# Performance work log

Hardware: AMD Instinct MI355X
Metric: run time of the kernel (lower is better)

The kernel has to match this reference:

```python
import jax, jax.numpy as jnp
import numpy as np

D_MODEL = 1024
NUM_HEADS = 16
D_K = D_MODEL // NUM_HEADS
B, S = 2, 2048


def setup_inputs() -> dict:
    key = jax.random.key(0)
    ks = jax.random.split(key, 11)
    lim = 1.0 / np.sqrt(D_MODEL)  # torch Linear default init range
    def lin(kw, kb):
        W = jax.random.uniform(kw, (D_MODEL, D_MODEL), jnp.float32, -lim, lim)
        b = jax.random.uniform(kb, (D_MODEL,), jnp.float32, -lim, lim)
        return W, b
    Wq, bq = lin(ks[0], ks[1])
    Wk, bk = lin(ks[2], ks[3])
    Wv, bv = lin(ks[4], ks[5])
    Wo, bo = lin(ks[6], ks[7])
    return {
        "Q": jax.random.normal(ks[8], (B, S, D_MODEL), jnp.float32),
        "K": jax.random.normal(ks[9], (B, S, D_MODEL), jnp.float32),
        "V": jax.random.normal(ks[10], (B, S, D_MODEL), jnp.float32),
        "Wq": Wq, "bq": bq, "Wk": Wk, "bk": bk,
        "Wv": Wv, "bv": bv, "Wo": Wo, "bo": bo,
        "validate": False,
    }


def _split_heads(x):
    b, s, _ = x.shape
    return x.reshape(b, s, NUM_HEADS, D_K).transpose(0, 2, 1, 3)  # [B,H,S,Dk]


def reference(Q, K, V, Wq, bq, Wk, bk, Wv, bv, Wo, bo, validate):
    # Linear projections (torch Linear: x @ W.T + b)
    q = _split_heads(Q @ Wq.T + bq)
    k = _split_heads(K @ Wk.T + bk)
    v = _split_heads(V @ Wv.T + bv)
    scale = 1.0 / jnp.sqrt(jnp.asarray(D_K, q.dtype))
    scores = jnp.einsum("bhqd,bhkd->bhqk", q, k) * scale  # [B,H,S,S]
    attn = jax.nn.softmax(scores, axis=-1)
    out = jnp.einsum("bhqk,bhkd->bhqd", attn, v)  # [B,H,S,Dk]
    out = out.transpose(0, 2, 1, 3).reshape(Q.shape[0], Q.shape[1], D_MODEL)
    return out @ Wo.T + bo
```

## Files before the change

### kernel.cpp

```cpp
#include <hip/hip_runtime.h>


typedef short bf16x8 __attribute__((ext_vector_type(8)));
typedef float f32x4 __attribute__((ext_vector_type(4)));

#define D_MODEL 1024
#define NHEAD 16
#define DK 64
#define BB 2
#define SS 2048
#define MROWS (BB * SS)
#define C1 0.18033688011112042f

__device__ __forceinline__ unsigned short f2bf(float f) {
  unsigned u = __builtin_bit_cast(unsigned, f);
  u += 0x7fffu + ((u >> 16) & 1u);
  return (unsigned short)(u >> 16);
}
__device__ __forceinline__ unsigned pack2(float a, float b) {
  return (unsigned)f2bf(a) | ((unsigned)f2bf(b) << 16);
}
__device__ __forceinline__ unsigned cvtpk(float lo, float hi) {
  unsigned r;
  asm("v_cvt_pk_bf16_f32 %0, %1, %2" : "=v"(r) : "v"(lo), "v"(hi));
  return r;
}
__device__ __forceinline__ float max3f(float a, float b, float c) {
  float d;
  asm("v_max3_f32 %0, %1, %2, %3" : "=v"(d) : "v"(a), "v"(b), "v"(c));
  return d;
}

typedef __attribute__((address_space(3))) unsigned int as3u;
typedef const __attribute__((address_space(1))) unsigned int as1u;
__device__ __forceinline__ void gload16(void* lds, const void* g) {
  __builtin_amdgcn_global_load_lds((as1u*)g, (as3u*)lds, 16, 0, 0);
}
__device__ __forceinline__ void waitv16() { asm volatile("s_waitcnt vmcnt(16)" ::: "memory"); }
__device__ __forceinline__ void waitv8()  { asm volatile("s_waitcnt vmcnt(8)"  ::: "memory"); }
__device__ __forceinline__ void waitv4()  { asm volatile("s_waitcnt vmcnt(4)"  ::: "memory"); }
__device__ __forceinline__ void waitv0()  { asm volatile("s_waitcnt vmcnt(0)"  ::: "memory"); }

struct CvtArgs {
  const float* s[7];
  unsigned short* d[7];
  int n8[7];
};

__global__ __launch_bounds__(256) void convert_bf16(CvtArgs a) {
  const int slot = blockIdx.y;
  const float* __restrict__ s = a.s[slot];
  unsigned short* __restrict__ d = a.d[slot];
  const int n8 = a.n8[slot];
  for (int i = blockIdx.x * 256 + threadIdx.x; i < n8; i += gridDim.x * 256) {
    const size_t off = (size_t)i * 8;
    const float4 v0 = *(const float4*)&s[off];
    const float4 v1 = *(const float4*)&s[off + 4];
    uint4 p;
    p.x = pack2(v0.x, v0.y); p.y = pack2(v0.z, v0.w);
    p.z = pack2(v1.x, v1.y); p.w = pack2(v1.z, v1.w);
    *(uint4*)&d[off] = p;
  }
}

template <int MODE>
__device__ __forceinline__ void gemm128(unsigned short* smem,
                                        const unsigned short* __restrict__ A,
                                        const unsigned short* __restrict__ B,
                                        const float* __restrict__ bias,
                                        float scale, int bm, int nb,
                                        float* __restrict__ Cf,
                                        unsigned short* __restrict__ Cb) {
  const int BUF = 2 * 128 * 64;
  const int tid = threadIdx.x;
  const int lane = tid & 63, w = tid >> 6;
  const int wm = w >> 1, wn = w & 1;
  const int l15 = lane & 15, l4 = lane >> 4;

  auto stage = [&](int slot, int k0) {
    unsigned short* As = smem + slot * BUF;
    unsigned short* Bs = As + 128 * 64;
#pragma unroll
    for (int i = 0; i < 4; ++i) {
      const int flat = i * 256 + tid;
      const int row = flat >> 3, g = flat & 7;
      const int gs = (g ^ (row & 7)) << 3;
      gload16(&As[flat * 8], &A[(size_t)(bm * 128 + row) * D_MODEL + k0 + gs]);
    }
#pragma unroll
    for (int i = 0; i < 4; ++i) {
      const int flat = i * 256 + tid;
      const int row = flat >> 3, g = flat & 7;
      const int gs = (g ^ (row & 7)) << 3;
      gload16(&Bs[flat * 8], &B[(size_t)(nb * 128 + row) * D_MODEL + k0 + gs]);
    }
  };

  f32x4 acc[4][4];
#pragma unroll
  for (int m = 0; m < 4; ++m)
#pragma unroll
    for (int n = 0; n < 4; ++n) acc[m][n] = (f32x4){0.f, 0.f, 0.f, 0.f};

  stage(0, 0);
  stage(1, 64);
#pragma unroll
  for (int t = 0; t < 16; ++t) {
    if (t + 2 < 16) stage((t + 2) % 3, (t + 2) * 64);
    if (t < 14) waitv16();
    else if (t == 14) waitv8();
    else waitv0();
    __builtin_amdgcn_s_barrier();
    unsigned short* As = smem + (t % 3) * BUF;
    unsigned short* Bs = As + 128 * 64;
#pragma unroll
    for (int kk = 0; kk < 2; ++kk) {
      bf16x8 af[4], bf[4];
#pragma unroll
      for (int m = 0; m < 4; ++m) {
        const int r = wm * 64 + m * 16 + l15;
        af[m] = *(const bf16x8*)&As[r * 64 + (((kk * 4 + l4) ^ (r & 7)) << 3)];
      }
#pragma unroll
      for (int n = 0; n < 4; ++n) {
        const int r = wn * 64 + n * 16 + l15;
        bf[n] = *(const bf16x8*)&Bs[r * 64 + (((kk * 4 + l4) ^ (r & 7)) << 3)];
      }
#pragma unroll
      for (int m = 0; m < 4; ++m)
#pragma unroll
        for (int n = 0; n < 4; ++n)
          acc[m][n] = __builtin_amdgcn_mfma_f32_16x16x32_bf16(af[m], bf[n], acc[m][n], 0, 0, 0);
    }
    __builtin_amdgcn_s_barrier();
  }

  if (MODE != 2) {
#pragma unroll
    for (int m = 0; m < 4; ++m)
#pragma unroll
      for (int n = 0; n < 4; ++n) {
        const int col = nb * 128 + wn * 64 + n * 16 + l15;
        const float bv = bias[col];
#pragma unroll
        for (int r = 0; r < 4; ++r) {
          const int row = bm * 128 + wm * 64 + m * 16 + l4 * 4 + r;
          const float v = (acc[m][n][r] + bv) * scale;
          if (MODE == 0) Cb[(size_t)row * D_MODEL + col] = f2bf(v);
          else           Cf[(size_t)row * D_MODEL + col] = v;
        }
      }
  } else {
    unsigned short* T = smem;
#pragma unroll
    for (int m = 0; m < 4; ++m)
#pragma unroll
      for (int n = 0; n < 4; ++n) {
        const int cl = wn * 64 + n * 16 + l15;
        const float bv = bias[nb * 128 + cl];
#pragma unroll
        for (int r = 0; r < 4; ++r) {
          const int rl = wm * 64 + m * 16 + l4 * 4 + r;
          const int byte = cl * 256 + ((((rl >> 3) ^ (cl & 7))) << 4) + ((rl & 7) << 1);
          *(unsigned short*)((char*)T + byte) = f2bf(acc[m][n][r] + bv);
        }
      }
    __syncthreads();
#pragma unroll
    for (int c = 0; c < 8; ++c) {
      const int chunk = c * 256 + tid;
      const int cl = chunk >> 4, rl0 = (chunk & 15) * 8;
      const int byte = cl * 256 + (((rl0 >> 3) ^ (cl & 7)) << 4);
      const uint4 val = *(const uint4*)((const char*)T + byte);
      const int gcol = nb * 128 + cl;
      const int bb = (bm * 128) >> 11;
      const int s = ((bm * 128) & 2047) + rl0;
      *(uint4*)&Cb[(size_t)(bb * 1024 + gcol) * SS + s] = val;
    }
  }
}

__global__ __launch_bounds__(256, 1) void gemm_qkv(
    const unsigned short* __restrict__ Xq, const unsigned short* __restrict__ Xk,
    const unsigned short* __restrict__ Xv,
    const unsigned short* __restrict__ Wq, const float* __restrict__ bq,
    const unsigned short* __restrict__ Wk, const float* __restrict__ bk,
    const unsigned short* __restrict__ Wv, const float* __restrict__ bv,
    unsigned short* __restrict__ q, unsigned short* __restrict__ k,
    unsigned short* __restrict__ vT) {
  __shared__ __align__(16) unsigned short smem[3 * 2 * 128 * 64];
  const int lin = blockIdx.x + 24 * blockIdx.y;
  const int swz = (lin % 8) * 96 + lin / 8;
  const int bn = swz % 24, bm = swz / 24;
  const int z = bn >> 3, nb = bn & 7;
  if (z < 2) {
    const unsigned short* X = z ? Xk : Xq;
    const unsigned short* W = z ? Wk : Wq;
    const float* bi = z ? bk : bq;
    unsigned short* O = z ? k : q;
    gemm128<0>(smem, X, W, bi, z ? 1.0f : C1, bm, nb, nullptr, O);
  } else {
    gemm128<2>(smem, Xv, Wv, bv, 1.0f, bm, nb, nullptr, vT);
  }
}

__global__ __launch_bounds__(256, 1) void gemm_o(const unsigned short* __restrict__ A,
                                                 const unsigned short* __restrict__ W,
                                                 const float* __restrict__ bi,
                                                 float* __restrict__ out) {
  __shared__ __align__(16) unsigned short smem[3 * 2 * 128 * 64];
  const int lin = blockIdx.x + 8 * blockIdx.y;
  const int swz = (lin % 8) * 32 + lin / 8;
  const int bn = swz % 8, bm = swz / 8;
  gemm128<1>(smem, A, W, bi, 1.0f, bm, bn, out, nullptr);
}

__global__ __launch_bounds__(256, 2) void attn_kernel(
    const unsigned short* __restrict__ Qp, const unsigned short* __restrict__ Kp,
    const unsigned short* __restrict__ vTp, unsigned short* __restrict__ Op) {
  __shared__ __align__(16) unsigned short Kt[3][64 * 64];
  __shared__ __align__(16) unsigned short Vt[3][64 * 64];
  __shared__ __align__(16) unsigned short Pt[4][32 * 64];
  const int tid = threadIdx.x;
  const int lane = tid & 63, w = tid >> 6;
  const int l15 = lane & 15, l4 = lane >> 4;
  const int bh = blockIdx.x;
  const int b = bh >> 4, h = bh & 15;
  const int qb = blockIdx.y;
  const size_t baseQ = (size_t)b * SS * D_MODEL + (size_t)h * DK;
  const size_t baseV = (size_t)(b * 1024 + h * 64) * SS;

  bf16x8 aq[2][2];
#pragma unroll
  for (int m = 0; m < 2; ++m) {
    const int qrow = qb * 128 + w * 32 + m * 16 + l15;
#pragma unroll
    for (int kk = 0; kk < 2; ++kk)
      aq[m][kk] = *(const bf16x8*)&Qp[baseQ + (size_t)qrow * D_MODEL + kk * 32 + l4 * 8];
  }

  const bf16x8 vone = {0x3F80, 0x3F80, 0x3F80, 0x3F80, 0x3F80, 0x3F80, 0x3F80, 0x3F80};

  float rm[2] = {-1e30f, -1e30f};
  f32x4 acc[2][5];
#pragma unroll
  for (int m = 0; m < 2; ++m)
#pragma unroll
    for (int d = 0; d < 5; ++d) acc[m][d] = (f32x4){0.f, 0.f, 0.f, 0.f};

  auto stage = [&](int buf, int kt) {
#pragma unroll
    for (int i = 0; i < 2; ++i) {
      const int flat = (w * 2 + i) * 64 + lane;
      const int row = flat >> 3, g = flat & 7;
      gload16(&Kt[buf][flat * 8],
              &Kp[baseQ + (size_t)(kt * 64 + row) * D_MODEL + ((g ^ (row & 7)) << 3)]);
    }
#pragma unroll
    for (int i = 0; i < 2; ++i) {
      const int flat = (w * 2 + i) * 64 + lane;
      const int row = flat >> 3, g = flat & 7;
      gload16(&Vt[buf][flat * 8],
              &vTp[baseV + (size_t)row * SS + kt * 64 + ((g ^ (row & 7)) << 3)]);
    }
  };

  stage(0, 0);
  stage(1, 1);
#pragma unroll 1
  for (int kt = 0; kt < SS / 64; ++kt) {
    const int bs = kt % 3;
    if (kt < SS / 64 - 2) {
      int bst = bs + 2; if (bst >= 3) bst -= 3;
      stage(bst, kt + 2);
    }
    if (kt < SS / 64 - 2) waitv8();
    else if (kt == SS / 64 - 2) waitv4();
    else waitv0();
    __builtin_amdgcn_s_barrier();

    f32x4 st[2][4];
#pragma unroll
    for (int m = 0; m < 2; ++m)
#pragma unroll
      for (int n = 0; n < 4; ++n) st[m][n] = (f32x4){0.f, 0.f, 0.f, 0.f};
#pragma unroll
    for (int kk = 0; kk < 2; ++kk) {
      bf16x8 kf[4];
#pragma unroll
      for (int n = 0; n < 4; ++n) {
        const int r = n * 16 + l15;
        kf[n] = *(const bf16x8*)&Kt[bs][r * 64 + (((kk * 4 + l4) ^ (r & 7)) << 3)];
      }
#pragma unroll
      for (int m = 0; m < 2; ++m)
#pragma unroll
        for (int n = 0; n < 4; ++n)
          st[m][n] = __builtin_amdgcn_mfma_f32_16x16x32_bf16(kf[n], aq[m][kk], st[m][n], 0, 0, 0);
    }

    float mx[2];
#pragma unroll
    for (int m = 0; m < 2; ++m) {
      const float a0 = max3f(st[m][0][0], st[m][0][1], st[m][0][2]);
      const float a1 = max3f(st[m][0][3], st[m][1][0], st[m][1][1]);
      const float a2 = max3f(st[m][1][2], st[m][1][3], st[m][2][0]);
      const float a3 = max3f(st[m][2][1], st[m][2][2], st[m][2][3]);
      const float a4 = max3f(st[m][3][0], st[m][3][1], st[m][3][2]);
      float v = fmaxf(max3f(a0, a1, a2), max3f(a3, a4, st[m][3][3]));
      v = fmaxf(v, __shfl_xor(v, 16));
      v = fmaxf(v, __shfl_xor(v, 32));
      mx[m] = v;
    }
    if (__any((mx[0] > rm[0] + 8.f) | (mx[1] > rm[1] + 8.f))) {
#pragma unroll
      for (int m = 0; m < 2; ++m) {
        const float nm = fmaxf(rm[m], mx[m]);
        const float alpha = exp2f(rm[m] - nm);
        rm[m] = nm;
#pragma unroll
        for (int r = 0; r < 4; ++r) {
          const float ar = __shfl(alpha, l4 * 4 + r);
#pragma unroll
          for (int d = 0; d < 5; ++d) acc[m][d][r] *= ar;
        }
      }
    }
#pragma unroll
    for (int m = 0; m < 2; ++m)
#pragma unroll
      for (int n = 0; n < 4; ++n)
#pragma unroll
        for (int r = 0; r < 4; ++r) st[m][n][r] = exp2f(st[m][n][r] - rm[m]);

#pragma unroll
    for (int m = 0; m < 2; ++m)
#pragma unroll
      for (int n = 0; n < 4; ++n)
#pragma unroll
        for (int c = 0; c < 2; ++c) {
          const int col = n * 16 + l4 * 4 + 2 * c;
          const int row = m * 16 + l15;
          const int sw = (((col >> 3) ^ (row & 7)) << 3) + (col & 7);
          *(unsigned*)&Pt[w][row * 64 + sw] = cvtpk(st[m][n][2 * c], st[m][n][2 * c + 1]);
        }

#pragma unroll
    for (int kk = 0; kk < 2; ++kk) {
      bf16x8 ap[2], vf[4];
#pragma unroll
      for (int m = 0; m < 2; ++m) {
        const int r = m * 16 + l15;
        ap[m] = *(const bf16x8*)&Pt[w][r * 64 + (((kk * 4 + l4) ^ (r & 7)) << 3)];
      }
#pragma unroll
      for (int d = 0; d < 4; ++d) {
        const int r = d * 16 + l15;
        vf[d] = *(const bf16x8*)&Vt[bs][r * 64 + (((kk * 4 + l4) ^ (r & 7)) << 3)];
      }
#pragma unroll
      for (int m = 0; m < 2; ++m) {
#pragma unroll
        for (int d = 0; d < 4; ++d)
          acc[m][d] = __builtin_amdgcn_mfma_f32_16x16x32_bf16(ap[m], vf[d], acc[m][d], 0, 0, 0);
        acc[m][4] = __builtin_amdgcn_mfma_f32_16x16x32_bf16(ap[m], vone, acc[m][4], 0, 0, 0);
      }
    }

    __builtin_amdgcn_s_barrier();
  }

#pragma unroll
  for (int m = 0; m < 2; ++m) {
    float inv[4];
#pragma unroll
    for (int r = 0; r < 4; ++r) inv[r] = 1.0f / acc[m][4][r];
#pragma unroll
    for (int d = 0; d < 4; ++d)
#pragma unroll
      for (int r = 0; r < 4; ++r) {
        const int orow = qb * 128 + w * 32 + m * 16 + l4 * 4 + r;
        Op[baseQ + (size_t)orow * D_MODEL + d * 16 + l15] = f2bf(acc[m][d][r] * inv[r]);
      }
  }
}

extern "C" void kernel_launch(void* const* d_in, const int* in_sizes, int n_in,
                              void* d_out, int out_size, void* d_ws, size_t ws_size,
                              hipStream_t stream) {
  const float* Qin = (const float*)d_in[0];
  const float* Kin = (const float*)d_in[1];
  const float* Vin = (const float*)d_in[2];
  const float* Wq = (const float*)d_in[3];
  const float* bq = (const float*)d_in[4];
  const float* Wk = (const float*)d_in[5];
  const float* bk = (const float*)d_in[6];
  const float* Wv = (const float*)d_in[7];
  const float* bv = (const float*)d_in[8];
  const float* Wo = (const float*)d_in[9];
  const float* bo = (const float*)d_in[10];
  float* out = (float*)d_out;

  const size_t NX = (size_t)MROWS * D_MODEL;
  const size_t NW = (size_t)D_MODEL * D_MODEL;
  unsigned short* ws = (unsigned short*)d_ws;
  unsigned short* q  = ws;
  unsigned short* k  = ws + NX;
  unsigned short* vT = ws + 2 * NX;
  unsigned short* Xq = ws + 3 * NX;
  unsigned short* Xk = ws + 4 * NX;
  unsigned short* Xv = ws + 5 * NX;
  unsigned short* wq = ws + 6 * NX;
  unsigned short* wk = wq + NW;
  unsigned short* wv = wk + NW;
  unsigned short* wo = wv + NW;
  unsigned short* ao = Xq;

  CvtArgs ca;
  ca.s[0] = Qin; ca.d[0] = Xq; ca.n8[0] = (int)(NX / 8);
  ca.s[1] = Kin; ca.d[1] = Xk; ca.n8[1] = (int)(NX / 8);
  ca.s[2] = Vin; ca.d[2] = Xv; ca.n8[2] = (int)(NX / 8);
  ca.s[3] = Wq;  ca.d[3] = wq; ca.n8[3] = (int)(NW / 8);
  ca.s[4] = Wk;  ca.d[4] = wk; ca.n8[4] = (int)(NW / 8);
  ca.s[5] = Wv;  ca.d[5] = wv; ca.n8[5] = (int)(NW / 8);
  ca.s[6] = Wo;  ca.d[6] = wo; ca.n8[6] = (int)(NW / 8);
  convert_bf16<<<dim3(1024, 7), 256, 0, stream>>>(ca);

  gemm_qkv<<<dim3(24, 32), 256, 0, stream>>>(
      Xq, Xk, Xv, wq, bq, wk, bk, wv, bv, q, k, vT);
  attn_kernel<<<dim3(BB * NHEAD, SS / 128), 256, 0, stream>>>(q, k, vT, ao);
  gemm_o<<<dim3(8, 32), 256, 0, stream>>>(ao, wo, bo, out);
}
```

Baseline: 237.3 us.

## Fuse fp32-to-bf16 activation conversion into QKV GEMM A-tile loads

```diff
diff --git a/kernel.cpp b/kernel.cpp
--- a/kernel.cpp
+++ b/kernel.cpp
@@ -36,22 +36,20 @@
 __device__ __forceinline__ void gload16(void* lds, const void* g) {
   __builtin_amdgcn_global_load_lds((as1u*)g, (as3u*)lds, 16, 0, 0);
 }
-__device__ __forceinline__ void waitv16() { asm volatile("s_waitcnt vmcnt(16)" ::: "memory"); }
 __device__ __forceinline__ void waitv8()  { asm volatile("s_waitcnt vmcnt(8)"  ::: "memory"); }
 __device__ __forceinline__ void waitv4()  { asm volatile("s_waitcnt vmcnt(4)"  ::: "memory"); }
 __device__ __forceinline__ void waitv0()  { asm volatile("s_waitcnt vmcnt(0)"  ::: "memory"); }
 
 struct CvtArgs {
-  const float* s[7];
-  unsigned short* d[7];
-  int n8[7];
+  const float* s[4];
+  unsigned short* d[4];
 };
 
-__global__ __launch_bounds__(256) void convert_bf16(CvtArgs a) {
+__global__ __launch_bounds__(256) void convert_w(CvtArgs a) {
   const int slot = blockIdx.y;
   const float* __restrict__ s = a.s[slot];
   unsigned short* __restrict__ d = a.d[slot];
-  const int n8 = a.n8[slot];
+  const int n8 = (D_MODEL * D_MODEL) / 8;
   for (int i = blockIdx.x * 256 + threadIdx.x; i < n8; i += gridDim.x * 256) {
     const size_t off = (size_t)i * 8;
     const float4 v0 = *(const float4*)&s[off];
@@ -64,37 +62,47 @@
 }
 
 template <int MODE>
-__device__ __forceinline__ void gemm128(unsigned short* smem,
-                                        const unsigned short* __restrict__ A,
-                                        const unsigned short* __restrict__ B,
-                                        const float* __restrict__ bias,
-                                        float scale, int bm, int nb,
-                                        float* __restrict__ Cf,
-                                        unsigned short* __restrict__ Cb) {
+__device__ __forceinline__ void gemm_qkv_core(unsigned short* smem,
+                                              const float* __restrict__ A,
+                                              const unsigned short* __restrict__ B,
+                                              const float* __restrict__ bias,
+                                              float scale, int bm, int nb,
+                                              unsigned short* __restrict__ Cb) {
   const int BUF = 2 * 128 * 64;
   const int tid = threadIdx.x;
   const int lane = tid & 63, w = tid >> 6;
   const int wm = w >> 1, wn = w & 1;
   const int l15 = lane & 15, l4 = lane >> 4;
 
-  auto stage = [&](int slot, int k0) {
-    unsigned short* As = smem + slot * BUF;
-    unsigned short* Bs = As + 128 * 64;
+  auto stageW = [&](unsigned short* Bs, int k0) {
 #pragma unroll
     for (int i = 0; i < 4; ++i) {
       const int flat = i * 256 + tid;
       const int row = flat >> 3, g = flat & 7;
-      const int gs = (g ^ (row & 7)) << 3;
-      gload16(&As[flat * 8], &A[(size_t)(bm * 128 + row) * D_MODEL + k0 + gs]);
-    }
+      gload16(&Bs[flat * 8], &B[(size_t)(nb * 128 + row) * D_MODEL + k0 + ((g ^ (row & 7)) << 3)]);
+    }
+  };
+  auto loadA = [&](float4 (&ar)[4][2], int k0) {
 #pragma unroll
     for (int i = 0; i < 4; ++i) {
       const int flat = i * 256 + tid;
       const int row = flat >> 3, g = flat & 7;
-      const int gs = (g ^ (row & 7)) << 3;
-      gload16(&Bs[flat * 8], &B[(size_t)(nb * 128 + row) * D_MODEL + k0 + gs]);
+      const float* src = &A[(size_t)(bm * 128 + row) * D_MODEL + k0 + g * 8];
+      ar[i][0] = *(const float4*)src;
+      ar[i][1] = *(const float4*)(src + 4);
     }
   };
+  auto writeA = [&](unsigned short* As, float4 (&ar)[4][2]) {
+#pragma unroll
+    for (int i = 0; i < 4; ++i) {
+      const int flat = i * 256 + tid;
+      const int row = flat >> 3, g = flat & 7;
+      uint4 p;
+      p.x = cvtpk(ar[i][0].x, ar[i][0].y); p.y = cvtpk(ar[i][0].z, ar[i][0].w);
+      p.z = cvtpk(ar[i][1].x, ar[i][1].y); p.w = cvtpk(ar[i][1].z, ar[i][1].w);
+      *(uint4*)&As[row * 64 + ((g ^ (row & 7)) << 3)] = p;
+    }
+  };
 
   f32x4 acc[4][4];
 #pragma unroll
@@ -102,17 +110,24 @@
 #pragma unroll
     for (int n = 0; n < 4; ++n) acc[m][n] = (f32x4){0.f, 0.f, 0.f, 0.f};
 
-  stage(0, 0);
-  stage(1, 64);
-#pragma unroll
+  float4 ar[4][2];
+  stageW(smem + 128 * 64, 0);
+  loadA(ar, 0);
+  waitv0();
+  writeA(smem, ar);
+  __syncthreads();
+
+  int cur = 0;
+#pragma unroll 1
   for (int t = 0; t < 16; ++t) {
-    if (t + 2 < 16) stage((t + 2) % 3, (t + 2) * 64);
-    if (t < 14) waitv16();
-    else if (t == 14) waitv8();
-    else waitv0();
-    __builtin_amdgcn_s_barrier();
-    unsigned short* As = smem + (t % 3) * BUF;
+    unsigned short* As = smem + cur * BUF;
     unsigned short* Bs = As + 128 * 64;
+    unsigned short* Asn = smem + (cur ^ 1) * BUF;
+    const bool more = (t + 1 < 16);
+    if (more) {
+      stageW(Asn + 128 * 64, (t + 1) * 64);
+      loadA(ar, (t + 1) * 64);
+    }
 #pragma unroll
     for (int kk = 0; kk < 2; ++kk) {
       bf16x8 af[4], bf[4];
@@ -132,10 +147,15 @@
         for (int n = 0; n < 4; ++n)
           acc[m][n] = __builtin_amdgcn_mfma_f32_16x16x32_bf16(af[m], bf[n], acc[m][n], 0, 0, 0);
     }
-    __builtin_amdgcn_s_barrier();
-  }
-
-  if (MODE != 2) {
+    if (more) {
+      waitv0();
+      writeA(Asn, ar);
+    }
+    __syncthreads();
+    cur ^= 1;
+  }
+
+  if (MODE == 0) {
 #pragma unroll
     for (int m = 0; m < 4; ++m)
 #pragma unroll
@@ -145,9 +165,7 @@
 #pragma unroll
         for (int r = 0; r < 4; ++r) {
           const int row = bm * 128 + wm * 64 + m * 16 + l4 * 4 + r;
-          const float v = (acc[m][n][r] + bv) * scale;
-          if (MODE == 0) Cb[(size_t)row * D_MODEL + col] = f2bf(v);
-          else           Cf[(size_t)row * D_MODEL + col] = v;
+          Cb[(size_t)row * D_MODEL + col] = f2bf((acc[m][n][r] + bv) * scale);
         }
       }
   } else {
@@ -180,39 +198,112 @@
   }
 }
 
-__global__ __launch_bounds__(256, 1) void gemm_qkv(
-    const unsigned short* __restrict__ Xq, const unsigned short* __restrict__ Xk,
-    const unsigned short* __restrict__ Xv,
+__global__ __launch_bounds__(256, 2) void gemm_qkv(
+    const float* __restrict__ Qin, const float* __restrict__ Kin,
+    const float* __restrict__ Vin,
     const unsigned short* __restrict__ Wq, const float* __restrict__ bq,
     const unsigned short* __restrict__ Wk, const float* __restrict__ bk,
     const unsigned short* __restrict__ Wv, const float* __restrict__ bv,
     unsigned short* __restrict__ q, unsigned short* __restrict__ k,
     unsigned short* __restrict__ vT) {
-  __shared__ __align__(16) unsigned short smem[3 * 2 * 128 * 64];
+  __shared__ __align__(16) unsigned short smem[2 * 2 * 128 * 64];
   const int lin = blockIdx.x + 24 * blockIdx.y;
   const int swz = (lin % 8) * 96 + lin / 8;
   const int bn = swz % 24, bm = swz / 24;
   const int z = bn >> 3, nb = bn & 7;
-  if (z < 2) {
-    const unsigned short* X = z ? Xk : Xq;
-    const unsigned short* W = z ? Wk : Wq;
-    const float* bi = z ? bk : bq;
-    unsigned short* O = z ? k : q;
-    gemm128<0>(smem, X, W, bi, z ? 1.0f : C1, bm, nb, nullptr, O);
+  if (z == 0) {
+    gemm_qkv_core<0>(smem, Qin, Wq, bq, C1, bm, nb, q);
+  } else if (z == 1) {
+    gemm_qkv_core<0>(smem, Kin, Wk, bk, 1.0f, bm, nb, k);
   } else {
-    gemm128<2>(smem, Xv, Wv, bv, 1.0f, bm, nb, nullptr, vT);
-  }
-}
-
-__global__ __launch_bounds__(256, 1) void gemm_o(const unsigned short* __restrict__ A,
+    gemm_qkv_core<2>(smem, Vin, Wv, bv, 1.0f, bm, nb, vT);
+  }
+}
+
+__global__ __launch_bounds__(256, 2) void gemm_o(const unsigned short* __restrict__ A,
                                                  const unsigned short* __restrict__ W,
                                                  const float* __restrict__ bi,
                                                  float* __restrict__ out) {
-  __shared__ __align__(16) unsigned short smem[3 * 2 * 128 * 64];
+  __shared__ __align__(16) unsigned short smem[2 * 2 * 128 * 64];
+  const int BUF = 2 * 128 * 64;
   const int lin = blockIdx.x + 8 * blockIdx.y;
   const int swz = (lin % 8) * 32 + lin / 8;
-  const int bn = swz % 8, bm = swz / 8;
-  gemm128<1>(smem, A, W, bi, 1.0f, bm, bn, out, nullptr);
+  const int nb = swz % 8, bm = swz / 8;
+  const int tid = threadIdx.x;
+  const int lane = tid & 63, w = tid >> 6;
+  const int wm = w >> 1, wn = w & 1;
+  const int l15 = lane & 15, l4 = lane >> 4;
+
+  auto stage = [&](unsigned short* dst, int k0) {
+    unsigned short* As = dst;
+    unsigned short* Bs = dst + 128 * 64;
+#pragma unroll
+    for (int i = 0; i < 4; ++i) {
+      const int flat = i * 256 + tid;
+      const int row = flat >> 3, g = flat & 7;
+      const int gs = (g ^ (row & 7)) << 3;
+      gload16(&As[flat * 8], &A[(size_t)(bm * 128 + row) * D_MODEL + k0 + gs]);
+    }
+#pragma unroll
+    for (int i = 0; i < 4; ++i) {
+      const int flat = i * 256 + tid;
+      const int row = flat >> 3, g = flat & 7;
+      const int gs = (g ^ (row & 7)) << 3;
+      gload16(&Bs[flat * 8], &W[(size_t)(nb * 128 + row) * D_MODEL + k0 + gs]);
+    }
+  };
+
+  f32x4 acc[4][4];
+#pragma unroll
+  for (int m = 0; m < 4; ++m)
+#pragma unroll
+    for (int n = 0; n < 4; ++n) acc[m][n] = (f32x4){0.f, 0.f, 0.f, 0.f};
+
+  stage(smem, 0);
+  int cur = 0;
+#pragma unroll 1
+  for (int t = 0; t < 16; ++t) {
+    if (t + 1 < 16) stage(smem + (cur ^ 1) * BUF, (t + 1) * 64);
+    if (t + 1 < 16) waitv8();
+    else waitv0();
+    __builtin_amdgcn_s_barrier();
+    unsigned short* As = smem + cur * BUF;
+    unsigned short* Bs = As + 128 * 64;
+#pragma unroll
+    for (int kk = 0; kk < 2; ++kk) {
+      bf16x8 af[4], bf[4];
+#pragma unroll
+      for (int m = 0; m < 4; ++m) {
+        const int r = wm * 64 + m * 16 + l15;
+        af[m] = *(const bf16x8*)&As[r * 64 + (((kk * 4 + l4) ^ (r & 7)) << 3)];
+      }
+#pragma unroll
+      for (int n = 0; n < 4; ++n) {
+        const int r = wn * 64 + n * 16 + l15;
+        bf[n] = *(const bf16x8*)&Bs[r * 64 + (((kk * 4 + l4) ^ (r & 7)) << 3)];
+      }
+#pragma unroll
+      for (int m = 0; m < 4; ++m)
+#pragma unroll
+        for (int n = 0; n < 4; ++n)
+          acc[m][n] = __builtin_amdgcn_mfma_f32_16x16x32_bf16(af[m], bf[n], acc[m][n], 0, 0, 0);
+    }
+    __builtin_amdgcn_s_barrier();
+    cur ^= 1;
+  }
+
+#pragma unroll
+  for (int m = 0; m < 4; ++m)
+#pragma unroll
+    for (int n = 0; n < 4; ++n) {
+      const int col = nb * 128 + wn * 64 + n * 16 + l15;
+      const float bv = bi[col];
+#pragma unroll
+      for (int r = 0; r < 4; ++r) {
+        const int row = bm * 128 + wm * 64 + m * 16 + l4 * 4 + r;
+        out[(size_t)row * D_MODEL + col] = acc[m][n][r] + bv;
+      }
+    }
 }
 
 __global__ __launch_bounds__(256, 2) void attn_kernel(
@@ -407,27 +498,21 @@
   unsigned short* q  = ws;
   unsigned short* k  = ws + NX;
   unsigned short* vT = ws + 2 * NX;
-  unsigned short* Xq = ws + 3 * NX;
-  unsigned short* Xk = ws + 4 * NX;
-  unsigned short* Xv = ws + 5 * NX;
-  unsigned short* wq = ws + 6 * NX;
+  unsigned short* ao = ws + 3 * NX;
+  unsigned short* wq = ws + 4 * NX;
   unsigned short* wk = wq + NW;
   unsigned short* wv = wk + NW;
   unsigned short* wo = wv + NW;
-  unsigned short* ao = Xq;
 
   CvtArgs ca;
-  ca.s[0] = Qin; ca.d[0] = Xq; ca.n8[0] = (int)(NX / 8);
-  ca.s[1] = Kin; ca.d[1] = Xk; ca.n8[1] = (int)(NX / 8);
-  ca.s[2] = Vin; ca.d[2] = Xv; ca.n8[2] = (int)(NX / 8);
-  ca.s[3] = Wq;  ca.d[3] = wq; ca.n8[3] = (int)(NW / 8);
-  ca.s[4] = Wk;  ca.d[4] = wk; ca.n8[4] = (int)(NW / 8);
-  ca.s[5] = Wv;  ca.d[5] = wv; ca.n8[5] = (int)(NW / 8);
-  ca.s[6] = Wo;  ca.d[6] = wo; ca.n8[6] = (int)(NW / 8);
-  convert_bf16<<<dim3(1024, 7), 256, 0, stream>>>(ca);
+  ca.s[0] = Wq; ca.d[0] = wq;
+  ca.s[1] = Wk; ca.d[1] = wk;
+  ca.s[2] = Wv; ca.d[2] = wv;
+  ca.s[3] = Wo; ca.d[3] = wo;
+  convert_w<<<dim3(128, 4), 256, 0, stream>>>(ca);
 
   gemm_qkv<<<dim3(24, 32), 256, 0, stream>>>(
-      Xq, Xk, Xv, wq, bq, wk, bk, wv, bv, q, k, vT);
+      Qin, Kin, Vin, wq, bq, wk, bk, wv, bv, q, k, vT);
   attn_kernel<<<dim3(BB * NHEAD, SS / 128), 256, 0, stream>>>(q, k, vT, ao);
   gemm_o<<<dim3(8, 32), 256, 0, stream>>>(ao, wo, bo, out);
 }
```

Measured after the change: 247.5 us. 4.3% more time.
